# Optimization experiments

Measured on AMD Instinct MI355X. Metric: run time of the kernel, lower is better.

Reference implementation:

```python
import jax, jax.numpy as jnp
import numpy as np

STRIDE = 1
PADDING = 1

def setup_inputs() -> dict:
    key = jax.random.key(0)
    k1, k2 = jax.random.split(key)
    x = jax.random.normal(k1, (32, 128, 56, 56), dtype=jnp.float32)
    weight = jax.random.normal(k2, (256, 128, 3, 3), dtype=jnp.float32) * 0.01
    bias = jnp.zeros((256,), dtype=jnp.float32)
    return {"x": x, "weight": weight, "bias": bias}

def reference(x, weight, bias):
    # Same math as unfold (im2col) + matmul conv: a standard 2D cross-correlation.
    # Expressed as lax.conv_general_dilated, the efficient implicit-GEMM form.
    out = jax.lax.conv_general_dilated(
        x, weight,
        window_strides=(STRIDE, STRIDE),
        padding=[(PADDING, PADDING), (PADDING, PADDING)],
        dimension_numbers=("NCHW", "OIHW", "NCHW"),
    )
    out = out + bias[None, :, None, None]
    return out
```

## Files before the change

kernel.cpp:

```cpp
#include <hip/hip_runtime.h>

typedef int   v4i __attribute__((ext_vector_type(4)));
typedef float v4f __attribute__((ext_vector_type(4)));
typedef unsigned short ushort_t;

#define NB 32
#define CI 128
#define HW 56
#define KOC 256
#define HP 58
#define MTOT (NB*HW*HW)
#define XP_ELEMS ((size_t)NB*HP*HP*CI)
#define XP_OFF_BYTES ((size_t)1<<20)

__device__ __forceinline__ unsigned short f2bf(float f) {
    unsigned int u = __builtin_bit_cast(unsigned int, f);
    u += 0x7fffu + ((u >> 16) & 1u);
    return (unsigned short)(u >> 16);
}

__device__ __forceinline__ void gload16(const void* g, void* l) {
    __builtin_amdgcn_global_load_lds(
        (const __attribute__((address_space(1))) void*)g,
        (__attribute__((address_space(3))) void*)l, 16, 0, 0);
}

__global__ void wt_bf16(const float* __restrict__ w, ushort_t* __restrict__ wb) {
    int t = blockIdx.x * 256 + threadIdx.x;
    if (t >= KOC * CI) return;
    const float* src = w + (size_t)t * 9;
    int ko = t >> 7, c = t & 127;
    #pragma unroll
    for (int rs = 0; rs < 9; ++rs)
        wb[(size_t)(rs * KOC + ko) * CI + c] = f2bf(src[rs]);
}

__global__ void pad_nhwc_bf16(const float* __restrict__ x, ushort_t* __restrict__ xp) {
    __shared__ ushort_t tile[HW][136];
    int b = blockIdx.x;
    int n = b / HW, h = b % HW;
    int tid = threadIdx.x;
    const float* xr = x + (size_t)n * CI * HW * HW + (size_t)h * HW;
    for (int idx = tid; idx < CI * HW; idx += 256) {
        int c = idx / HW, w = idx % HW;
        tile[w][c] = f2bf(xr[(size_t)c * (HW * HW) + w]);
    }
    __syncthreads();
    ushort_t* xpr = xp + ((size_t)(n * HP + (h + 1)) * HP + 1) * CI;
    for (int idx = tid; idx < (HW * CI) / 8; idx += 256) {
        int w = idx >> 4, c8 = (idx & 15) * 8;
        *reinterpret_cast<uint4*>(xpr + (size_t)w * CI + c8) =
            *reinterpret_cast<const uint4*>(&tile[w][c8]);
    }
}

__global__ void border_zero(ushort_t* __restrict__ xp) {
    int t = blockIdx.x * 256 + threadIdx.x;
    if (t >= NB * 228 * 16) return;
    int c16 = t & 15;
    int p = (t >> 4) % 228;
    int n = t / (228 * 16);
    int h, wc;
    if (p < 58)       { h = 0;               wc = p; }
    else if (p < 116) { h = 57;              wc = p - 58; }
    else { int q = p - 116; h = 1 + (q >> 1); wc = (q & 1) * 57; }
    size_t off = ((size_t)(n * HP + h) * HP + wc) * CI + (size_t)c16 * 8;
    uint4 z; z.x = z.y = z.z = z.w = 0u;
    *reinterpret_cast<uint4*>(xp + off) = z;
}

__global__ __launch_bounds__(256, 2) void conv_mfma(
    const ushort_t* __restrict__ xp,
    const ushort_t* __restrict__ wb,
    const float* __restrict__ bias,
    float* __restrict__ out)
{
    __shared__ alignas(16) ushort_t sW[2][128 * 64];
    __shared__ alignas(16) ushort_t sX[2][128 * 64];

    const int tid  = threadIdx.x;
    const int lane = tid & 63;
    const int wv   = tid >> 6;
    const int wko  = wv >> 1, wm = wv & 1;
    const int m0   = blockIdx.x * 128;
    const int ko0  = blockIdx.y * 128;

    const int srow   = lane >> 3;
    const int schunk = (lane & 7) ^ srow;
    const ushort_t* wsrc[4];
    const ushort_t* xsrc[4];
    #pragma unroll
    for (int j = 0; j < 4; ++j) {
        int row = wv * 32 + j * 8 + srow;
        wsrc[j] = wb + (size_t)(ko0 + row) * CI + schunk * 8;
        int m = m0 + row;
        int n = m / 3136, tt = m % 3136, oh = tt / 56, ow = tt % 56;
        xsrc[j] = xp + ((size_t)(n * HP + oh) * HP + ow) * CI + schunk * 8;
    }

    const int lm = lane & 15, lk = lane >> 4, l7 = lane & 7;
    int offA[4][2], offB[4][2];
    #pragma unroll
    for (int a = 0; a < 4; ++a)
        #pragma unroll
        for (int h = 0; h < 2; ++h) {
            int rowA = wko * 64 + a * 16 + lm;
            int rowB = wm  * 64 + a * 16 + lm;
            int s = (h * 4 + lk) ^ l7;
            offA[a][h] = rowA * 64 + s * 8;
            offB[a][h] = rowB * 64 + s * 8;
        }

    v4f acc[4][4];
    const v4f vzero = {0.f, 0.f, 0.f, 0.f};
    #pragma unroll
    for (int a = 0; a < 4; ++a)
        #pragma unroll
        for (int b = 0; b < 4; ++b) acc[a][b] = vzero;

    auto stage = [&](int buf, int t) {
        int rs = t >> 1;
        int r  = (rs * 11) >> 5;
        int s  = rs - r * 3;
        int ch = (t & 1) << 6;
        int woff = rs * (KOC * CI) + ch;
        int xoff = (r * HP + s) * CI + ch;
        char* dW = (char*)&sW[0][0] + buf * 16384 + wv * 4096;
        char* dX = (char*)&sX[0][0] + buf * 16384 + wv * 4096;
        #pragma unroll
        for (int j = 0; j < 4; ++j) {
            gload16(wsrc[j] + woff, dW + j * 1024);
            gload16(xsrc[j] + xoff, dX + j * 1024);
        }
    };

    stage(0, 0);
    __syncthreads();

    for (int t = 0; t < 18; ++t) {
        int cur = t & 1;
        if (t < 17) stage(cur ^ 1, t + 1);

        const ushort_t* bW = &sW[cur][0];
        const ushort_t* bX = &sX[cur][0];
        #pragma unroll
        for (int h = 0; h < 2; ++h) {
            v4i af[4], bf[4];
            #pragma unroll
            for (int a = 0; a < 4; ++a)
                af[a] = *reinterpret_cast<const v4i*>(bW + offA[a][h]);
            #pragma unroll
            for (int b = 0; b < 4; ++b)
                bf[b] = *reinterpret_cast<const v4i*>(bX + offB[b][h]);
            __builtin_amdgcn_s_setprio(1);
            #pragma unroll
            for (int a = 0; a < 4; ++a)
                #pragma unroll
                for (int b = 0; b < 4; ++b)
                    asm volatile("v_mfma_f32_16x16x32_bf16 %0, %1, %2, %0"
                                 : "+v"(acc[a][b]) : "v"(af[a]), "v"(bf[b]));
            __builtin_amdgcn_s_setprio(0);
        }
        __syncthreads();
    }

    asm volatile("s_nop 7\n\ts_nop 7\n\ts_nop 7"
        : "+v"(acc[0][0]), "+v"(acc[0][1]), "+v"(acc[0][2]), "+v"(acc[0][3]),
          "+v"(acc[1][0]), "+v"(acc[1][1]), "+v"(acc[1][2]), "+v"(acc[1][3]),
          "+v"(acc[2][0]), "+v"(acc[2][1]), "+v"(acc[2][2]), "+v"(acc[2][3]),
          "+v"(acc[3][0]), "+v"(acc[3][1]), "+v"(acc[3][2]), "+v"(acc[3][3]));

    const int koBase = ko0 + wko * 64 + (lane >> 4) * 4;
    float bv[4][4];
    #pragma unroll
    for (int a = 0; a < 4; ++a)
        #pragma unroll
        for (int r = 0; r < 4; ++r)
            bv[a][r] = bias[koBase + a * 16 + r];

    #pragma unroll
    for (int b = 0; b < 4; ++b) {
        int mcol = m0 + wm * 64 + b * 16 + (lane & 15);
        int n = mcol / 3136, t4 = mcol % 3136, oh = t4 / 56, ow = t4 % 56;
        size_t obase = (size_t)n * (KOC * 3136) + (size_t)oh * 56 + ow;
        #pragma unroll
        for (int a = 0; a < 4; ++a) {
            int kk = koBase + a * 16;
            #pragma unroll
            for (int r = 0; r < 4; ++r)
                out[obase + (size_t)(kk + r) * 3136] = acc[a][b][r] + bv[a][r];
        }
    }
}

__global__ void conv_naive(const float* __restrict__ x, const float* __restrict__ w,
                           const float* __restrict__ bias, float* __restrict__ out) {
    int idx = blockIdx.x * 256 + threadIdx.x;
    if (idx >= NB * KOC * HW * HW) return;
    int ow = idx % 56, t = idx / 56, oh = t % 56, t2 = t / 56, ko = t2 % 256, n = t2 / 256;
    float accv = bias[ko];
    for (int c = 0; c < CI; ++c)
        for (int r = 0; r < 3; ++r) {
            int ih = oh - 1 + r;
            if (ih < 0 || ih >= HW) continue;
            for (int s = 0; s < 3; ++s) {
                int iw = ow - 1 + s;
                if (iw < 0 || iw >= HW) continue;
                accv += x[((size_t)(n * CI + c) * HW + ih) * HW + iw] *
                        w[((size_t)(ko * CI + c) * 3 + r) * 3 + s];
            }
        }
    out[idx] = accv;
}

extern "C" void kernel_launch(void* const* d_in, const int* in_sizes, int n_in,
                              void* d_out, int out_size, void* d_ws, size_t ws_size,
                              hipStream_t stream) {
    const float* x    = (const float*)d_in[0];
    const float* w    = (const float*)d_in[1];
    const float* bias = (const float*)d_in[2];
    float* out = (float*)d_out;

    size_t need = XP_OFF_BYTES + XP_ELEMS * 2;
    if (ws_size < need) {
        int tot = NB * KOC * HW * HW;
        conv_naive<<<dim3((tot + 255) / 256), dim3(256), 0, stream>>>(x, w, bias, out);
        return;
    }

    ushort_t* wbp = (ushort_t*)d_ws;
    ushort_t* xpd = (ushort_t*)((char*)d_ws + XP_OFF_BYTES);

    border_zero<<<dim3((NB * 228 * 16 + 255) / 256), dim3(256), 0, stream>>>(xpd);
    wt_bf16<<<dim3((KOC * CI + 255) / 256), dim3(256), 0, stream>>>(w, wbp);
    pad_nhwc_bf16<<<dim3(NB * HW), dim3(256), 0, stream>>>(x, xpd);

    dim3 grid(MTOT / 128, 2);
    conv_mfma<<<grid, dim3(256), 0, stream>>>(xpd, wbp, bias, out);
}
```

Measured before the change: 115.4 us.

## Use 256x256 output tiles with 8-wave blocks and phased LDS pipeline

Makes each conv block cover all 256 output channels and 256 output positions, using 512 threads and 128KB of LDS. The K loop is split into 8 half-tile phases per step, each issuing its next global-to-LDS load before the MFMAs and guarded by explicit vmcnt waits and raw barriers. Bias is loaded with vector loads. The aim is more operand reuse per LDS load and better overlap of loads with MFMA. In exchange, one block per CU likely limits occupancy, and the grid of 392 blocks may leave part of the last wave of CUs idle.

Result: faster. 104.2 us (-9.7%).

```diff
diff --git a/kernel.cpp b/kernel.cpp
--- a/kernel.cpp
+++ b/kernel.cpp
@@ -69,126 +69,155 @@
     *reinterpret_cast<uint4*>(xp + off) = z;
 }
 
-__global__ __launch_bounds__(256, 2) void conv_mfma(
+
+#define BAR() asm volatile("s_barrier" ::: "memory")
+#define VMW(n) asm volatile("s_waitcnt vmcnt(" #n ")" ::: "memory")
+
+#define PHASE(BUF, KH, MH, STAGE_STMT, VMSTMT) do {                               \
+    const char* pbase = lds + (BUF) * 65536 + (KH) * 16384;                       \
+    if ((MH) == 0) {                                                              \
+        _Pragma("unroll")                                                         \
+        for (int a = 0; a < 8; ++a)                                               \
+            af[a] = *reinterpret_cast<const v4i*>(pbase + aoff[a]);               \
+    }                                                                             \
+    v4i bf0 = *reinterpret_cast<const v4i*>(pbase + boff[(MH)*2]);                \
+    v4i bf1 = *reinterpret_cast<const v4i*>(pbase + boff[(MH)*2+1]);              \
+    STAGE_STMT;                                                                   \
+    VMSTMT;                                                                       \
+    BAR();                                                                        \
+    __builtin_amdgcn_s_setprio(1);                                                \
+    _Pragma("unroll")                                                             \
+    for (int a = 0; a < 8; ++a) {                                                 \
+        asm volatile("v_mfma_f32_16x16x32_bf16 %0, %1, %2, %0"                    \
+                     : "+v"(acc[a][(MH)*2])   : "v"(af[a]), "v"(bf0));            \
+        asm volatile("v_mfma_f32_16x16x32_bf16 %0, %1, %2, %0"                    \
+                     : "+v"(acc[a][(MH)*2+1]) : "v"(af[a]), "v"(bf1));            \
+    }                                                                             \
+    __builtin_amdgcn_s_setprio(0);                                                \
+    BAR();                                                                        \
+} while (0)
+
+__global__ __launch_bounds__(512, 2) void conv_mfma(
     const ushort_t* __restrict__ xp,
     const ushort_t* __restrict__ wb,
     const float* __restrict__ bias,
     float* __restrict__ out)
 {
-    __shared__ alignas(16) ushort_t sW[2][128 * 64];
-    __shared__ alignas(16) ushort_t sX[2][128 * 64];
+    __shared__ alignas(16) char lds[131072];
 
     const int tid  = threadIdx.x;
     const int lane = tid & 63;
     const int wv   = tid >> 6;
-    const int wko  = wv >> 1, wm = wv & 1;
-    const int m0   = blockIdx.x * 128;
-    const int ko0  = blockIdx.y * 128;
-
-    const int srow   = lane >> 3;
-    const int schunk = (lane & 7) ^ srow;
-    const ushort_t* wsrc[4];
-    const ushort_t* xsrc[4];
-    #pragma unroll
-    for (int j = 0; j < 4; ++j) {
-        int row = wv * 32 + j * 8 + srow;
-        wsrc[j] = wb + (size_t)(ko0 + row) * CI + schunk * 8;
-        int m = m0 + row;
-        int n = m / 3136, tt = m % 3136, oh = tt / 56, ow = tt % 56;
-        xsrc[j] = xp + ((size_t)(n * HP + oh) * HP + ow) * CI + schunk * 8;
-    }
-
-    const int lm = lane & 15, lk = lane >> 4, l7 = lane & 7;
-    int offA[4][2], offB[4][2];
-    #pragma unroll
-    for (int a = 0; a < 4; ++a)
-        #pragma unroll
-        for (int h = 0; h < 2; ++h) {
-            int rowA = wko * 64 + a * 16 + lm;
-            int rowB = wm  * 64 + a * 16 + lm;
-            int s = (h * 4 + lk) ^ l7;
-            offA[a][h] = rowA * 64 + s * 8;
-            offB[a][h] = rowB * 64 + s * 8;
-        }
-
-    v4f acc[4][4];
+    const int wko2 = wv >> 2;
+    const int wm4  = wv & 3;
+    const int m0   = blockIdx.x * 256;
+    const int lm = lane & 15, lk = lane >> 4;
+
+    const int srow = tid >> 2;
+    const int sc   = (tid & 3) ^ ((tid >> 3) & 3);
+    const size_t wA0 = (size_t)srow * CI + sc * 8;
+    const size_t wA1 = (size_t)(srow + 128) * CI + sc * 8;
+    size_t xB0, xB1;
+    {
+        int mm = m0 + srow;
+        int n = mm / 3136, tt = mm % 3136, oh = tt / 56, ow = tt % 56;
+        xB0 = ((size_t)(n * HP + oh) * HP + ow) * CI + sc * 8;
+        mm = m0 + 128 + srow;
+        n = mm / 3136; tt = mm % 3136; oh = tt / 56; ow = tt % 56;
+        xB1 = ((size_t)(n * HP + oh) * HP + ow) * CI + sc * 8;
+    }
+
+    auto stageA = [&](int buf, int kh, int kt) {
+        int rs = kt >> 1, ch = (kt & 1) << 6;
+        size_t g = (size_t)rs * (KOC * CI) + ch + kh * 32;
+        char* d = lds + buf * 65536 + kh * 16384 + wv * 1024;
+        gload16(wb + wA0 + g, d);
+        gload16(wb + wA1 + g, d + 8192);
+    };
+    auto stageB = [&](int buf, int kh, int kt) {
+        int rs = kt >> 1, ch = (kt & 1) << 6;
+        int r = (rs * 11) >> 5, s = rs - r * 3;
+        size_t g = (size_t)(r * HP + s) * CI + ch + kh * 32;
+        char* d = lds + buf * 65536 + 32768 + kh * 16384 + wv * 1024;
+        gload16(xp + xB0 + g, d);
+        gload16(xp + xB1 + g, d + 8192);
+    };
+
+    int aoff[8], boff[4];
+    #pragma unroll
+    for (int a = 0; a < 8; ++a) {
+        int row = wko2 * 128 + a * 16 + lm;
+        aoff[a] = row * 64 + ((lk ^ ((row >> 1) & 3)) * 16);
+    }
+    #pragma unroll
+    for (int bb = 0; bb < 4; ++bb) {
+        int row = wm4 * 64 + bb * 16 + lm;
+        boff[bb] = 32768 + row * 64 + ((lk ^ ((row >> 1) & 3)) * 16);
+    }
+
+    v4f acc[8][4];
     const v4f vzero = {0.f, 0.f, 0.f, 0.f};
     #pragma unroll
-    for (int a = 0; a < 4; ++a)
+    for (int a = 0; a < 8; ++a)
         #pragma unroll
         for (int b = 0; b < 4; ++b) acc[a][b] = vzero;
 
-    auto stage = [&](int buf, int t) {
-        int rs = t >> 1;
-        int r  = (rs * 11) >> 5;
-        int s  = rs - r * 3;
-        int ch = (t & 1) << 6;
-        int woff = rs * (KOC * CI) + ch;
-        int xoff = (r * HP + s) * CI + ch;
-        char* dW = (char*)&sW[0][0] + buf * 16384 + wv * 4096;
-        char* dX = (char*)&sX[0][0] + buf * 16384 + wv * 4096;
-        #pragma unroll
-        for (int j = 0; j < 4; ++j) {
-            gload16(wsrc[j] + woff, dW + j * 1024);
-            gload16(xsrc[j] + xoff, dX + j * 1024);
-        }
-    };
-
-    stage(0, 0);
-    __syncthreads();
-
-    for (int t = 0; t < 18; ++t) {
-        int cur = t & 1;
-        if (t < 17) stage(cur ^ 1, t + 1);
-
-        const ushort_t* bW = &sW[cur][0];
-        const ushort_t* bX = &sX[cur][0];
-        #pragma unroll
-        for (int h = 0; h < 2; ++h) {
-            v4i af[4], bf[4];
-            #pragma unroll
-            for (int a = 0; a < 4; ++a)
-                af[a] = *reinterpret_cast<const v4i*>(bW + offA[a][h]);
-            #pragma unroll
-            for (int b = 0; b < 4; ++b)
-                bf[b] = *reinterpret_cast<const v4i*>(bX + offB[b][h]);
-            __builtin_amdgcn_s_setprio(1);
-            #pragma unroll
-            for (int a = 0; a < 4; ++a)
-                #pragma unroll
-                for (int b = 0; b < 4; ++b)
-                    asm volatile("v_mfma_f32_16x16x32_bf16 %0, %1, %2, %0"
-                                 : "+v"(acc[a][b]) : "v"(af[a]), "v"(bf[b]));
-            __builtin_amdgcn_s_setprio(0);
-        }
-        __syncthreads();
-    }
-
-    asm volatile("s_nop 7\n\ts_nop 7\n\ts_nop 7"
+    v4i af[8];
+
+    stageA(0, 0, 0); stageB(0, 0, 0); stageA(0, 1, 0); stageB(0, 1, 0);
+    stageA(1, 0, 1); stageB(1, 0, 1);
+    VMW(8);
+    BAR();
+
+    for (int t = 0; t < 8; ++t) {
+        int e2 = 2 * t;
+        PHASE(0, 0, 0, stageA(1, 1, e2 + 1), VMW(8));
+        PHASE(0, 0, 1, stageB(1, 1, e2 + 1), VMW(8));
+        PHASE(0, 1, 0, stageA(0, 0, e2 + 2), VMW(8));
+        PHASE(0, 1, 1, stageB(0, 0, e2 + 2), VMW(8));
+        PHASE(1, 0, 0, stageA(0, 1, e2 + 2), VMW(8));
+        PHASE(1, 0, 1, stageB(0, 1, e2 + 2), VMW(8));
+        PHASE(1, 1, 0, stageA(1, 0, e2 + 3), VMW(8));
+        PHASE(1, 1, 1, stageB(1, 0, e2 + 3), VMW(8));
+    }
+
+    PHASE(0, 0, 0, stageA(1, 1, 17), VMW(8));
+    PHASE(0, 0, 1, stageB(1, 1, 17), VMW(8));
+    PHASE(0, 1, 0, (void)0, VMW(8));
+    PHASE(0, 1, 1, (void)0, VMW(4));
+    PHASE(1, 0, 0, (void)0, VMW(4));
+    PHASE(1, 0, 1, (void)0, VMW(0));
+    PHASE(1, 1, 0, (void)0, VMW(0));
+    PHASE(1, 1, 1, (void)0, VMW(0));
+
+    asm volatile("s_nop 7\n\ts_nop 7"
         : "+v"(acc[0][0]), "+v"(acc[0][1]), "+v"(acc[0][2]), "+v"(acc[0][3]),
           "+v"(acc[1][0]), "+v"(acc[1][1]), "+v"(acc[1][2]), "+v"(acc[1][3]),
           "+v"(acc[2][0]), "+v"(acc[2][1]), "+v"(acc[2][2]), "+v"(acc[2][3]),
           "+v"(acc[3][0]), "+v"(acc[3][1]), "+v"(acc[3][2]), "+v"(acc[3][3]));
-
-    const int koBase = ko0 + wko * 64 + (lane >> 4) * 4;
-    float bv[4][4];
-    #pragma unroll
-    for (int a = 0; a < 4; ++a)
-        #pragma unroll
-        for (int r = 0; r < 4; ++r)
-            bv[a][r] = bias[koBase + a * 16 + r];
-
-    #pragma unroll
-    for (int b = 0; b < 4; ++b) {
-        int mcol = m0 + wm * 64 + b * 16 + (lane & 15);
+    asm volatile("s_nop 7\n\ts_nop 7"
+        : "+v"(acc[4][0]), "+v"(acc[4][1]), "+v"(acc[4][2]), "+v"(acc[4][3]),
+          "+v"(acc[5][0]), "+v"(acc[5][1]), "+v"(acc[5][2]), "+v"(acc[5][3]),
+          "+v"(acc[6][0]), "+v"(acc[6][1]), "+v"(acc[6][2]), "+v"(acc[6][3]),
+          "+v"(acc[7][0]), "+v"(acc[7][1]), "+v"(acc[7][2]), "+v"(acc[7][3]));
+
+    const int koB = wko2 * 128 + lk * 4;
+    v4f bv[8];
+    #pragma unroll
+    for (int a = 0; a < 8; ++a)
+        bv[a] = *reinterpret_cast<const v4f*>(bias + koB + a * 16);
+
+    #pragma unroll
+    for (int bb = 0; bb < 4; ++bb) {
+        int mcol = m0 + wm4 * 64 + bb * 16 + lm;
         int n = mcol / 3136, t4 = mcol % 3136, oh = t4 / 56, ow = t4 % 56;
         size_t obase = (size_t)n * (KOC * 3136) + (size_t)oh * 56 + ow;
         #pragma unroll
-        for (int a = 0; a < 4; ++a) {
-            int kk = koBase + a * 16;
+        for (int a = 0; a < 8; ++a) {
+            int kk = koB + a * 16;
             #pragma unroll
             for (int r = 0; r < 4; ++r)
-                out[obase + (size_t)(kk + r) * 3136] = acc[a][b][r] + bv[a][r];
+                out[obase + (size_t)(kk + r) * 3136] = acc[a][bb][r] + bv[a][r];
         }
     }
 }
@@ -235,6 +264,5 @@
     wt_bf16<<<dim3((KOC * CI + 255) / 256), dim3(256), 0, stream>>>(w, wbp);
     pad_nhwc_bf16<<<dim3(NB * HW), dim3(256), 0, stream>>>(x, xpd);
 
-    dim3 grid(MTOT / 128, 2);
-    conv_mfma<<<grid, dim3(256), 0, stream>>>(xpd, wbp, bias, out);
-}
+    conv_mfma<<<dim3(MTOT / 256), dim3(512), 0, stream>>>(xpd, wbp, bias, out);
+}
```

## Shrink LDS tile to single-buffered K=32 and raise occupancy with swizzled 1D grid

Applied to the files above, without the earlier changes.

The conv MFMA kernel drops its double-buffered 64-wide K tiles for single-buffered 32-wide tiles (16 KB LDS instead of 64 KB) and raises launch bounds to 4 blocks per CU. Latency is meant to be hidden by more resident waves rather than software pipelining. The grid becomes 1D with a chunked remap so blocks sharing an M tile and its two KO tiles run close together, improving L2 reuse. It also uses a new XOR swizzle for the smaller tile and vector bias loads. The trade-off is twice as many barriers and no overlap of loads with MFMA inside a block.

Measured after the change: 105.2 us. 8.8% less time.

```diff
diff --git a/kernel.cpp b/kernel.cpp
--- a/kernel.cpp
+++ b/kernel.cpp
@@ -69,47 +69,51 @@
     *reinterpret_cast<uint4*>(xp + off) = z;
 }
 
-__global__ __launch_bounds__(256, 2) void conv_mfma(
+
+__global__ __launch_bounds__(256, 4) void conv_mfma(
     const ushort_t* __restrict__ xp,
     const ushort_t* __restrict__ wb,
     const float* __restrict__ bias,
     float* __restrict__ out)
 {
-    __shared__ alignas(16) ushort_t sW[2][128 * 64];
-    __shared__ alignas(16) ushort_t sX[2][128 * 64];
+    __shared__ alignas(16) ushort_t sA[128 * 32];
+    __shared__ alignas(16) ushort_t sB[128 * 32];
 
     const int tid  = threadIdx.x;
     const int lane = tid & 63;
     const int wv   = tid >> 6;
     const int wko  = wv >> 1, wm = wv & 1;
-    const int m0   = blockIdx.x * 128;
-    const int ko0  = blockIdx.y * 128;
-
-    const int srow   = lane >> 3;
-    const int schunk = (lane & 7) ^ srow;
-    const ushort_t* wsrc[4];
-    const ushort_t* xsrc[4];
-    #pragma unroll
-    for (int j = 0; j < 4; ++j) {
-        int row = wv * 32 + j * 8 + srow;
-        wsrc[j] = wb + (size_t)(ko0 + row) * CI + schunk * 8;
-        int m = m0 + row;
-        int n = m / 3136, tt = m % 3136, oh = tt / 56, ow = tt % 56;
-        xsrc[j] = xp + ((size_t)(n * HP + oh) * HP + ow) * CI + schunk * 8;
-    }
-
-    const int lm = lane & 15, lk = lane >> 4, l7 = lane & 7;
-    int offA[4][2], offB[4][2];
-    #pragma unroll
-    for (int a = 0; a < 4; ++a)
-        #pragma unroll
-        for (int h = 0; h < 2; ++h) {
-            int rowA = wko * 64 + a * 16 + lm;
-            int rowB = wm  * 64 + a * 16 + lm;
-            int s = (h * 4 + lk) ^ l7;
-            offA[a][h] = rowA * 64 + s * 8;
-            offB[a][h] = rowB * 64 + s * 8;
-        }
+    const int bid   = blockIdx.x;
+    const int chunk = (bid & 7) * 196 + (bid >> 3);
+    const int mt = chunk >> 1, kt = chunk & 1;
+    const int m0 = mt * 128, ko0 = kt * 128;
+    const int lm = lane & 15, lk = lane >> 4;
+
+    const int sc   = (lane & 3) ^ ((lane >> 3) & 3);
+    const int row0 = wv * 16 + (lane >> 2);
+    const size_t wS0 = (size_t)(ko0 + row0) * CI + sc * 8;
+    const size_t wS1 = (size_t)(ko0 + 64 + row0) * CI + sc * 8;
+    size_t xS0, xS1;
+    {
+        int mm = m0 + row0;
+        int n = mm / 3136, tt = mm % 3136, oh = tt / 56, ow = tt % 56;
+        xS0 = ((size_t)(n * HP + oh) * HP + ow) * CI + sc * 8;
+        mm = m0 + 64 + row0;
+        n = mm / 3136; tt = mm % 3136; oh = tt / 56; ow = tt % 56;
+        xS1 = ((size_t)(n * HP + oh) * HP + ow) * CI + sc * 8;
+    }
+
+    int aoffE[4], boffE[4];
+    #pragma unroll
+    for (int a = 0; a < 4; ++a) {
+        int row = wko * 64 + a * 16 + lm;
+        aoffE[a] = row * 32 + (lk ^ ((row >> 1) & 3)) * 8;
+    }
+    #pragma unroll
+    for (int b = 0; b < 4; ++b) {
+        int row = wm * 64 + b * 16 + lm;
+        boffE[b] = row * 32 + (lk ^ ((row >> 1) & 3)) * 8;
+    }
 
     v4f acc[4][4];
     const v4f vzero = {0.f, 0.f, 0.f, 0.f};
@@ -118,49 +122,37 @@
         #pragma unroll
         for (int b = 0; b < 4; ++b) acc[a][b] = vzero;
 
-    auto stage = [&](int buf, int t) {
-        int rs = t >> 1;
-        int r  = (rs * 11) >> 5;
-        int s  = rs - r * 3;
-        int ch = (t & 1) << 6;
-        int woff = rs * (KOC * CI) + ch;
-        int xoff = (r * HP + s) * CI + ch;
-        char* dW = (char*)&sW[0][0] + buf * 16384 + wv * 4096;
-        char* dX = (char*)&sX[0][0] + buf * 16384 + wv * 4096;
-        #pragma unroll
-        for (int j = 0; j < 4; ++j) {
-            gload16(wsrc[j] + woff, dW + j * 1024);
-            gload16(xsrc[j] + xoff, dX + j * 1024);
-        }
-    };
-
-    stage(0, 0);
-    __syncthreads();
-
-    for (int t = 0; t < 18; ++t) {
-        int cur = t & 1;
-        if (t < 17) stage(cur ^ 1, t + 1);
-
-        const ushort_t* bW = &sW[cur][0];
-        const ushort_t* bX = &sX[cur][0];
-        #pragma unroll
-        for (int h = 0; h < 2; ++h) {
-            v4i af[4], bf[4];
-            #pragma unroll
-            for (int a = 0; a < 4; ++a)
-                af[a] = *reinterpret_cast<const v4i*>(bW + offA[a][h]);
+    char* dA = (char*)sA + wv * 1024;
+    char* dB = (char*)sB + wv * 1024;
+
+    for (int it = 0; it < 36; ++it) {
+        int rs = it >> 2, coff = (it & 3) * 32;
+        int r  = (rs * 11) >> 5, s = rs - r * 3;
+        size_t woff = (size_t)rs * (KOC * CI) + coff;
+        size_t xoff = (size_t)(r * HP + s) * CI + coff;
+
+        gload16(wb + wS0 + woff, dA);
+        gload16(wb + wS1 + woff, dA + 4096);
+        gload16(xp + xS0 + xoff, dB);
+        gload16(xp + xS1 + xoff, dB + 4096);
+        __syncthreads();
+
+        v4i af[4], bf[4];
+        #pragma unroll
+        for (int a = 0; a < 4; ++a)
+            af[a] = *reinterpret_cast<const v4i*>(&sA[aoffE[a]]);
+        #pragma unroll
+        for (int b = 0; b < 4; ++b)
+            bf[b] = *reinterpret_cast<const v4i*>(&sB[boffE[b]]);
+
+        __builtin_amdgcn_s_setprio(1);
+        #pragma unroll
+        for (int a = 0; a < 4; ++a)
             #pragma unroll
             for (int b = 0; b < 4; ++b)
-                bf[b] = *reinterpret_cast<const v4i*>(bX + offB[b][h]);
-            __builtin_amdgcn_s_setprio(1);
-            #pragma unroll
-            for (int a = 0; a < 4; ++a)
-                #pragma unroll
-                for (int b = 0; b < 4; ++b)
-                    asm volatile("v_mfma_f32_16x16x32_bf16 %0, %1, %2, %0"
-                                 : "+v"(acc[a][b]) : "v"(af[a]), "v"(bf[b]));
-            __builtin_amdgcn_s_setprio(0);
-        }
+                asm volatile("v_mfma_f32_16x16x32_bf16 %0, %1, %2, %0"
+                             : "+v"(acc[a][b]) : "v"(af[a]), "v"(bf[b]));
+        __builtin_amdgcn_s_setprio(0);
         __syncthreads();
     }
 
@@ -170,25 +162,23 @@
           "+v"(acc[2][0]), "+v"(acc[2][1]), "+v"(acc[2][2]), "+v"(acc[2][3]),
           "+v"(acc[3][0]), "+v"(acc[3][1]), "+v"(acc[3][2]), "+v"(acc[3][3]));
 
-    const int koBase = ko0 + wko * 64 + (lane >> 4) * 4;
-    float bv[4][4];
+    const int koB = ko0 + wko * 64 + lk * 4;
+    v4f bv[4];
     #pragma unroll
     for (int a = 0; a < 4; ++a)
-        #pragma unroll
-        for (int r = 0; r < 4; ++r)
-            bv[a][r] = bias[koBase + a * 16 + r];
-
-    #pragma unroll
-    for (int b = 0; b < 4; ++b) {
-        int mcol = m0 + wm * 64 + b * 16 + (lane & 15);
+        bv[a] = *reinterpret_cast<const v4f*>(bias + koB + a * 16);
+
+    #pragma unroll
+    for (int bb = 0; bb < 4; ++bb) {
+        int mcol = m0 + wm * 64 + bb * 16 + lm;
         int n = mcol / 3136, t4 = mcol % 3136, oh = t4 / 56, ow = t4 % 56;
         size_t obase = (size_t)n * (KOC * 3136) + (size_t)oh * 56 + ow;
         #pragma unroll
         for (int a = 0; a < 4; ++a) {
-            int kk = koBase + a * 16;
+            int kk = koB + a * 16;
             #pragma unroll
             for (int r = 0; r < 4; ++r)
-                out[obase + (size_t)(kk + r) * 3136] = acc[a][b][r] + bv[a][r];
+                out[obase + (size_t)(kk + r) * 3136] = acc[a][bb][r] + bv[a][r];
         }
     }
 }
@@ -235,6 +225,5 @@
     wt_bf16<<<dim3((KOC * CI + 255) / 256), dim3(256), 0, stream>>>(w, wbp);
     pad_nhwc_bf16<<<dim3(NB * HW), dim3(256), 0, stream>>>(x, xpd);
 
-    dim3 grid(MTOT / 128, 2);
-    conv_mfma<<<grid, dim3(256), 0, stream>>>(xpd, wbp, bias, out);
-}
+    conv_mfma<<<dim3((MTOT / 128) * 2), dim3(256), 0, stream>>>(xpd, wbp, bias, out);
+}
```
